# Performance work log

Measured on AMD Instinct MI355X. Metric: run time of the kernel, lower is better.

Reference implementation:

```python
import jax, jax.numpy as jnp
import numpy as np

M, N, D = 16384, 128, 2048  # actions, question tokens, ExpSet.dim


def setup_inputs() -> dict:
    key = jax.random.key(0)
    ks = jax.random.split(key, 6)
    s1 = 1.0 / np.sqrt(2 * D)  # torch Linear default init bounds
    s2 = 1.0 / np.sqrt(D)
    return {
        "action_embedding": jax.random.normal(ks[0], (M, D), jnp.float32),
        "question_t": jax.random.normal(ks[1], (N, D), jnp.float32),
        "history_t": jax.random.normal(ks[2], (D,), jnp.float32),
        "W1": jax.random.uniform(ks[3], (D, 2 * D), jnp.float32, -s1, s1),
        "b1": jnp.zeros((D,), jnp.float32),
        "W2": jax.random.uniform(ks[4], (D, D), jnp.float32, -s2, s2),
        "b2": jnp.zeros((D,), jnp.float32),
    }


def reference(action_embedding, question_t, history_t, W1, b1, W2, b2):
    # Attention: each action (query) attends over the n question tokens.
    # Equivalent to expand->attend->sum in the torch code, but without
    # materializing the [m, n, d] expanded tensor.
    scores = action_embedding @ question_t.T              # [M, N]
    attn = jax.nn.softmax(scores, axis=1)                 # softmax over tokens
    question = attn @ question_t                          # [M, D] (attended + summed)

    # Perceptron(2d -> d -> d) on cat([history, question])
    hist = jnp.broadcast_to(history_t, (action_embedding.shape[0], history_t.shape[0]))
    qh = jnp.concatenate([hist, question], axis=1)        # [M, 2D]
    h = jax.nn.relu(qh @ W1.T + b1)                       # [M, D]
    qwh = h @ W2.T + b2                                   # [M, D]

    # Elementwise dot with action embeddings, softmax over actions.
    semantic_scores = jnp.sum(qwh * action_embedding, axis=1)  # [M]
    return jax.nn.softmax(semantic_scores, axis=0)
```

## Files before the change

kernel.cpp:

```cpp
#include <hip/hip_runtime.h>
#include <hip/hip_bf16.h>


typedef _Float16 f16;
typedef __attribute__((ext_vector_type(8))) _Float16 half8;
typedef __attribute__((ext_vector_type(4))) _Float16 half4_t;
typedef __attribute__((ext_vector_type(4))) float f32x4;

#define GLL(gp, lp)                                                              \
  __builtin_amdgcn_global_load_lds(                                              \
      (const __attribute__((address_space(1))) void*)(gp),                       \
      (__attribute__((address_space(3))) void*)(lp), 16, 0, 0)

#define WAITN(n)                                                                 \
  do {                                                                           \
    asm volatile("s_waitcnt vmcnt(" #n ")" ::: "memory");                        \
    __builtin_amdgcn_sched_barrier(0);                                           \
  } while (0)

template <int NT, int LDA, int LDB>
__device__ __forceinline__ void kloop1(const f16* __restrict__ A,
                                       const f16* __restrict__ B,
                                       f16* __restrict__ SM,
                                       f32x4 (&acc)[4][4],
                                       int lane, int wv, int wm, int wn) {
  static_assert(NT >= 4, "depth-3 pipeline needs NT >= 4");
  const int f = lane & 15, kk = lane >> 4;
  const int cS = (lane & 7) ^ (lane >> 3);
  const int kkS = (cS & 3) * 8;
  const int rS = 2 * (lane >> 3) + (cS >> 2);
  const size_t offA0 = (size_t)(16 * (wv * 2 + 0) + rS) * LDA + kkS;
  const size_t offA1 = (size_t)(16 * (wv * 2 + 1) + rS) * LDA + kkS;
  const size_t offB0 = (size_t)(16 * (wv * 2 + 0) + rS) * LDB + kkS;
  const size_t offB1 = (size_t)(16 * (wv * 2 + 1) + rS) * LDB + kkS;
  const int Ld0 = (wv * 2 + 0) * 512, Ld1 = (wv * 2 + 1) * 512;

  int aoff[4], boff[4];
  #pragma unroll
  for (int mf = 0; mf < 4; ++mf) {
    const int R = wm + mf * 16 + f;
    const int c2 = (((R & 1) << 2) | kk) ^ ((R >> 1) & 7);
    aoff[mf] = (R >> 1) * 64 + c2 * 8;
  }
  #pragma unroll
  for (int nf = 0; nf < 4; ++nf) {
    const int R = wn + nf * 16 + f;
    const int c2 = (((R & 1) << 2) | kk) ^ ((R >> 1) & 7);
    boff[nf] = (R >> 1) * 64 + c2 * 8;
  }

  auto STAGE = [&](int set, int kt) {
    f16* base = SM + set * 8192;
    GLL(A + offA0 + kt, base + Ld0);
    GLL(A + offA1 + kt, base + Ld1);
    GLL(B + offB0 + kt, base + 4096 + Ld0);
    GLL(B + offB1 + kt, base + 4096 + Ld1);
  };
  auto COMPUTE = [&](int set) {
    const f16* p = SM + set * 8192;
    half8 a[4], b[4];
    #pragma unroll
    for (int mf = 0; mf < 4; ++mf) a[mf] = *(const half8*)&p[aoff[mf]];
    #pragma unroll
    for (int nf = 0; nf < 4; ++nf) b[nf] = *(const half8*)&p[4096 + boff[nf]];
    __builtin_amdgcn_s_setprio(1);
    #pragma unroll
    for (int mf = 0; mf < 4; ++mf)
      #pragma unroll
      for (int nf = 0; nf < 4; ++nf)
        acc[mf][nf] = __builtin_amdgcn_mfma_f32_16x16x32_f16(a[mf], b[nf], acc[mf][nf], 0, 0, 0);
    __builtin_amdgcn_s_setprio(0);
  };

  STAGE(0, 0);
  STAGE(1, 32);
  STAGE(2, 64);
  #pragma unroll 1
  for (int t = 0; t < NT - 3; ++t) {
    STAGE((t + 3) & 3, (t + 3) * 32);
    WAITN(12);
    __builtin_amdgcn_s_barrier();
    COMPUTE(t & 3);
    __builtin_amdgcn_s_barrier();
  }
  WAITN(8);
  __builtin_amdgcn_s_barrier();
  COMPUTE((NT - 3) & 3);
  __builtin_amdgcn_s_barrier();
  WAITN(4);
  __builtin_amdgcn_s_barrier();
  COMPUTE((NT - 2) & 3);
  __builtin_amdgcn_s_barrier();
  WAITN(0);
  __builtin_amdgcn_s_barrier();
  COMPUTE((NT - 1) & 3);
  __builtin_amdgcn_s_barrier();
}

template <int NT, int LDA, int LDB>
__device__ __forceinline__ void kloop256(const f16* __restrict__ A,
                                         const f16* __restrict__ B,
                                         f16* __restrict__ SM,
                                         f32x4 (&acc)[8][4],
                                         int lane, int wv, int wm, int wn) {
  static_assert(NT >= 4, "pipeline needs NT >= 4");
  const int f = lane & 15, kk = lane >> 4;
  const int cS = (lane & 7) ^ (lane >> 3);
  const int kkS = (cS & 3) * 8;
  const int rS = 2 * (lane >> 3) + (cS >> 2);
  const size_t offA0 = (size_t)(16 * (wv * 2 + 0) + rS) * LDA + kkS;
  const size_t offA1 = (size_t)(16 * (wv * 2 + 1) + rS) * LDA + kkS;
  const size_t offB0 = (size_t)(16 * (wv * 2 + 0) + rS) * LDB + kkS;
  const size_t offB1 = (size_t)(16 * (wv * 2 + 1) + rS) * LDB + kkS;
  const int Ld0 = (wv * 2 + 0) * 512, Ld1 = (wv * 2 + 1) * 512;

  int aoff[8], boff[4];
  #pragma unroll
  for (int mf = 0; mf < 8; ++mf) {
    const int R = wm + mf * 16 + f;
    const int c2 = (((R & 1) << 2) | kk) ^ ((R >> 1) & 7);
    aoff[mf] = (R >> 1) * 64 + c2 * 8;
  }
  #pragma unroll
  for (int nf = 0; nf < 4; ++nf) {
    const int R = wn + nf * 16 + f;
    const int c2 = (((R & 1) << 2) | kk) ^ ((R >> 1) & 7);
    boff[nf] = (R >> 1) * 64 + c2 * 8;
  }

  auto STAGE = [&](int set, int kt) {
    f16* base = SM + set * 16384;
    GLL(A + offA0 + kt, base + Ld0);
    GLL(A + offA1 + kt, base + Ld1);
    GLL(B + offB0 + kt, base + 8192 + Ld0);
    GLL(B + offB1 + kt, base + 8192 + Ld1);
  };
  auto COMPUTE = [&](int set) {
    const f16* p = SM + set * 16384;
    half8 a[8], b[4];
    #pragma unroll
    for (int mf = 0; mf < 8; ++mf) a[mf] = *(const half8*)&p[aoff[mf]];
    #pragma unroll
    for (int nf = 0; nf < 4; ++nf) b[nf] = *(const half8*)&p[8192 + boff[nf]];
    __builtin_amdgcn_s_setprio(1);
    #pragma unroll
    for (int mf = 0; mf < 8; ++mf)
      #pragma unroll
      for (int nf = 0; nf < 4; ++nf)
        acc[mf][nf] = __builtin_amdgcn_mfma_f32_16x16x32_f16(a[mf], b[nf], acc[mf][nf], 0, 0, 0);
    __builtin_amdgcn_s_setprio(0);
  };

  STAGE(0, 0);
  STAGE(1, 32);
  int cs = 0;
  #pragma unroll 1
  for (int t = 0; t < NT - 2; ++t) {
    int ss = cs + 2; if (ss >= 3) ss -= 3;
    STAGE(ss, (t + 2) * 32);
    WAITN(8);
    __builtin_amdgcn_s_barrier();
    COMPUTE(cs);
    __builtin_amdgcn_s_barrier();
    ++cs; if (cs == 3) cs = 0;
  }
  WAITN(4);
  __builtin_amdgcn_s_barrier();
  COMPUTE(cs);
  __builtin_amdgcn_s_barrier();
  ++cs; if (cs == 3) cs = 0;
  WAITN(0);
  __builtin_amdgcn_s_barrier();
  COMPUTE(cs);
  __builtin_amdgcn_s_barrier();
}


__global__ __launch_bounds__(256) void c_kernel(const float* __restrict__ W1,
                                                const float* __restrict__ b1,
                                                const float* __restrict__ hist,
                                                float* __restrict__ c) {
  const int wave = threadIdx.x >> 6, lane = threadIdx.x & 63;
  const int j = blockIdx.x * 4 + wave;
  const float* row = W1 + (size_t)j * 4096;
  float s = 0.f;
  #pragma unroll 2
  for (int kq = lane; kq < 512; kq += 64) {
    const float4 w = *(const float4*)&row[kq * 4];
    const float4 h = *(const float4*)&hist[kq * 4];
    s += w.x * h.x + w.y * h.y + w.z * h.z + w.w * h.w;
  }
  #pragma unroll
  for (int mask = 1; mask < 64; mask <<= 1) s += __shfl_xor(s, mask);
  if (lane == 0) c[j] = s + b1[j];
}

__device__ __forceinline__ half4_t f16hi4(const float4 v) {
  half4_t h;
  h.x = (f16)v.x; h.y = (f16)v.y; h.z = (f16)v.z; h.w = (f16)v.w;
  return h;
}

__global__ __launch_bounds__(256) void prep_AQ(const float* __restrict__ A,
                                               const float* __restrict__ Q,
                                               const float* __restrict__ b2,
                                               f16* __restrict__ Af,
                                               f16* __restrict__ Qf,
                                               float* __restrict__ ab2) {
  const int wv = threadIdx.x >> 6, lane = threadIdx.x & 63;
  if (blockIdx.x < 4096) {
    const size_t row = (size_t)blockIdx.x * 4 + wv;
    const float* ar = A + row * 2048;
    float dot = 0.f;
    #pragma unroll 2
    for (int c0 = 0; c0 < 2048; c0 += 256) {
      const int col = c0 + lane * 4;
      const float4 v = *(const float4*)&ar[col];
      const float4 bb = *(const float4*)&b2[col];
      dot += v.x * bb.x + v.y * bb.y + v.z * bb.z + v.w * bb.w;
      *(half4_t*)&Af[row * 2048 + col] = f16hi4(v);
    }
    #pragma unroll
    for (int mask = 1; mask < 64; mask <<= 1) dot += __shfl_xor(dot, mask);
    if (lane == 0) ab2[row] = dot;
  } else {
    const size_t row = (size_t)(blockIdx.x - 4096) * 4 + wv;
    const float* qr = Q + row * 2048;
    #pragma unroll 2
    for (int c0 = 0; c0 < 2048; c0 += 256) {
      const int col = c0 + lane * 4;
      const float4 v = *(const float4*)&qr[col];
      *(half4_t*)&Qf[row * 2048 + col] = f16hi4(v);
    }
  }
}

__global__ __launch_bounds__(256) void transpose_f16(const float* __restrict__ src,
                                                     int R, int C,
                                                     f16* __restrict__ dst) {
  __shared__ float T[64][65];
  const int c0 = blockIdx.x * 64, r0 = blockIdx.y * 64;
  const int t = threadIdx.x;
  {
    const int rl = t >> 4, cl = (t & 15) * 4;
    #pragma unroll
    for (int ii = 0; ii < 4; ++ii) {
      const float4 v = *(const float4*)&src[(size_t)(r0 + rl + ii * 16) * C + c0 + cl];
      T[rl + ii * 16][cl + 0] = v.x; T[rl + ii * 16][cl + 1] = v.y;
      T[rl + ii * 16][cl + 2] = v.z; T[rl + ii * 16][cl + 3] = v.w;
    }
  }
  __syncthreads();
  const int cc = t >> 2, rr0 = (t & 3) * 16;
  f16 u[16];
  #pragma unroll
  for (int k = 0; k < 16; ++k) u[k] = (f16)T[rr0 + k][cc];
  f16* ph = dst + (size_t)(c0 + cc) * R + r0 + rr0;
  #pragma unroll
  for (int k4 = 0; k4 < 4; ++k4)
    *(half4_t*)&ph[k4 * 4] = *(half4_t*)&u[k4 * 4];
}

template <int BM, int TM>
__global__ __launch_bounds__(256) void gemm_bt_f16(const float* __restrict__ A,
                                                   const float* __restrict__ B,
                                                   f16* __restrict__ C,
                                                   int K, int lda, int ldb, int ldc) {
  constexpr int BN = 64, BK = 32;
  constexpr int ASTR = BM + 12, BSTR = BN + 4;
  __shared__ float As[BK][ASTR];
  __shared__ float Bs[BK][BSTR];
  const int tid = threadIdx.x;
  const int tx = tid & 15, ty = tid >> 4;
  const int m0 = ty * TM, n0 = tx * 4;
  const size_t bm = (size_t)blockIdx.x * BM, bn = (size_t)blockIdx.y * BN;
  const float* Ab = A + bm * lda;
  const float* Bb = B + bn * ldb;
  float acc[TM][4];
  #pragma unroll
  for (int i = 0; i < TM; ++i)
    #pragma unroll
    for (int j = 0; j < 4; ++j) acc[i][j] = 0.f;
  for (int kt = 0; kt < K; kt += BK) {
    #pragma unroll
    for (int it = 0; it < BM * BK / 4 / 256; ++it) {
      const int idx = it * 256 + tid;
      const int row = idx >> 3, kq = idx & 7;
      const float4 v = *(const float4*)&Ab[(size_t)row * lda + kt + kq * 4];
      As[kq * 4 + 0][row] = v.x; As[kq * 4 + 1][row] = v.y;
      As[kq * 4 + 2][row] = v.z; As[kq * 4 + 3][row] = v.w;
    }
    #pragma unroll
    for (int it = 0; it < BN * BK / 4 / 256; ++it) {
      const int idx = it * 256 + tid;
      const int row = idx >> 3, kq = idx & 7;
      const float4 v = *(const float4*)&Bb[(size_t)row * ldb + kt + kq * 4];
      Bs[kq * 4 + 0][row] = v.x; Bs[kq * 4 + 1][row] = v.y;
      Bs[kq * 4 + 2][row] = v.z; Bs[kq * 4 + 3][row] = v.w;
    }
    __syncthreads();
    #pragma unroll
    for (int k = 0; k < BK; ++k) {
      float av[TM];
      #pragma unroll
      for (int i = 0; i < TM; ++i) av[i] = As[k][m0 + i];
      const float4 b = *(const float4*)&Bs[k][n0];
      const float bv[4] = {b.x, b.y, b.z, b.w};
      #pragma unroll
      for (int i = 0; i < TM; ++i)
        #pragma unroll
        for (int j = 0; j < 4; ++j) acc[i][j] = fmaf(av[i], bv[j], acc[i][j]);
    }
    __syncthreads();
  }
  #pragma unroll
  for (int i = 0; i < TM; ++i) {
    f16* crow = C + (bm + m0 + i) * (size_t)ldc + bn + n0;
    half4_t h;
    h.x = (f16)acc[i][0]; h.y = (f16)acc[i][1];
    h.z = (f16)acc[i][2]; h.w = (f16)acc[i][3];
    *(half4_t*)crow = h;
  }
}

__global__ __launch_bounds__(256, 2) void s_attn(const f16* __restrict__ Af,
                                                 const f16* __restrict__ Qf,
                                                 f16* __restrict__ at) {
  __shared__ f16 SM[32768];
  const int tid = threadIdx.x, lane = tid & 63, wv = tid >> 6;
  const int wm = (wv >> 1) * 64, wn = (wv & 1) * 64;
  const int f = lane & 15, kk = lane >> 4;
  const size_t bm = (size_t)blockIdx.x * 128;

  f32x4 acc[4][4];
  #pragma unroll
  for (int mf = 0; mf < 4; ++mf)
    #pragma unroll
    for (int nf = 0; nf < 4; ++nf) acc[mf][nf] = 0.f;

  kloop1<64, 2048, 2048>(Af + bm * 2048, Qf, SM, acc, lane, wv, wm, wn);

  float* sred = (float*)SM;
  float* ssum = sred + 256;
  const int rowbase = wm + kk * 4;
  float rmax[4][4];
  #pragma unroll
  for (int mf = 0; mf < 4; ++mf)
    #pragma unroll
    for (int r = 0; r < 4; ++r) {
      float m4 = fmaxf(fmaxf(acc[mf][0][r], acc[mf][1][r]),
                       fmaxf(acc[mf][2][r], acc[mf][3][r]));
      m4 = fmaxf(m4, __shfl_xor(m4, 1));
      m4 = fmaxf(m4, __shfl_xor(m4, 2));
      m4 = fmaxf(m4, __shfl_xor(m4, 4));
      m4 = fmaxf(m4, __shfl_xor(m4, 8));
      rmax[mf][r] = m4;
    }
  if (f == 0) {
    #pragma unroll
    for (int mf = 0; mf < 4; ++mf)
      #pragma unroll
      for (int r = 0; r < 4; ++r)
        sred[(rowbase + mf * 16 + r) * 2 + (wv & 1)] = rmax[mf][r];
  }
  __syncthreads();
  #pragma unroll
  for (int mf = 0; mf < 4; ++mf)
    #pragma unroll
    for (int r = 0; r < 4; ++r) {
      const int row = rowbase + mf * 16 + r;
      rmax[mf][r] = fmaxf(sred[row * 2], sred[row * 2 + 1]);
    }
  float rsum[4][4];
  #pragma unroll
  for (int mf = 0; mf < 4; ++mf)
    #pragma unroll
    for (int r = 0; r < 4; ++r) {
      float s = 0.f;
      #pragma unroll
      for (int nf = 0; nf < 4; ++nf) {
        acc[mf][nf][r] = __expf(acc[mf][nf][r] - rmax[mf][r]);
        s += acc[mf][nf][r];
      }
      s += __shfl_xor(s, 1);
      s += __shfl_xor(s, 2);
      s += __shfl_xor(s, 4);
      s += __shfl_xor(s, 8);
      rsum[mf][r] = s;
    }
  if (f == 0) {
    #pragma unroll
    for (int mf = 0; mf < 4; ++mf)
      #pragma unroll
      for (int r = 0; r < 4; ++r)
        ssum[(rowbase + mf * 16 + r) * 2 + (wv & 1)] = rsum[mf][r];
  }
  __syncthreads();
  #pragma unroll
  for (int mf = 0; mf < 4; ++mf)
    #pragma unroll
    for (int r = 0; r < 4; ++r) {
      const int row = rowbase + mf * 16 + r;
      const float inv = 1.0f / (ssum[row * 2] + ssum[row * 2 + 1]);
      const size_t orow = (bm + row) * 128;
      #pragma unroll
      for (int nf = 0; nf < 4; ++nf)
        at[orow + wn + nf * 16 + f] = (f16)(acc[mf][nf][r] * inv);
    }
}

__global__ __launch_bounds__(256, 2) void h_kernel(const f16* __restrict__ at,
                                                   const f16* __restrict__ QWt,
                                                   const float* __restrict__ cvec,
                                                   f16* __restrict__ H) {
  __shared__ f16 SM[32768];
  const int tid = threadIdx.x, lane = tid & 63, wv = tid >> 6;
  const int wm = (wv >> 1) * 64, wn = (wv & 1) * 64;
  const int f = lane & 15, kk = lane >> 4;
  const size_t bm = (size_t)(blockIdx.x & 127) * 128;
  const size_t bn = (size_t)(blockIdx.x >> 7) * 128;

  f32x4 acc[4][4];
  #pragma unroll
  for (int mf = 0; mf < 4; ++mf)
    #pragma unroll
    for (int nf = 0; nf < 4; ++nf) acc[mf][nf] = 0.f;

  kloop1<4, 128, 128>(at + bm * 128, QWt + bn * 128, SM, acc, lane, wv, wm, wn);

  float ccv[4];
  #pragma unroll
  for (int nf = 0; nf < 4; ++nf) ccv[nf] = cvec[bn + wn + nf * 16 + f];
  #pragma unroll
  for (int mf = 0; mf < 4; ++mf)
    #pragma unroll
    for (int r = 0; r < 4; ++r) {
      const size_t row = bm + wm + mf * 16 + kk * 4 + r;
      #pragma unroll
      for (int nf = 0; nf < 4; ++nf)
        H[row * 2048 + bn + wn + nf * 16 + f] =
            (f16)fmaxf(acc[mf][nf][r] + ccv[nf], 0.f);
    }
}

__global__ __launch_bounds__(512, 1) void fused_g(
    const f16* __restrict__ Af, const f16* __restrict__ H,
    const f16* __restrict__ W2t, float* __restrict__ partial) {
  extern __shared__ f16 SM[];
  const int tid = threadIdx.x, lane = tid & 63, wv = tid >> 6;
  const int wm = (wv >> 2) * 128, wn = (wv & 3) * 64;
  const int f = lane & 15, kk = lane >> 4;
  const int lin = blockIdx.x;
  const int sid = (lin & 7) * 64 + (lin >> 3);
  const int bmI = sid & 63, bnI = sid >> 6;
  const size_t bm = (size_t)bmI * 256;
  const size_t bn = (size_t)bnI * 256;

  f32x4 acc[8][4];
  #pragma unroll
  for (int mf = 0; mf < 8; ++mf)
    #pragma unroll
    for (int nf = 0; nf < 4; ++nf) acc[mf][nf] = 0.f;

  kloop256<64, 2048, 2048>(Af + bm * 2048, W2t + bn * 2048, SM, acc, lane, wv, wm, wn);

  float part[8][4];
  #pragma unroll
  for (int mf = 0; mf < 8; ++mf)
    #pragma unroll
    for (int r = 0; r < 4; ++r) {
      const size_t hrow = (bm + wm + mf * 16 + kk * 4 + r) * 2048 + bn + wn + f;
      float s = 0.f;
      #pragma unroll
      for (int nf = 0; nf < 4; ++nf)
        s += (float)H[hrow + nf * 16] * acc[mf][nf][r];
      part[mf][r] = s;
    }
  #pragma unroll
  for (int mf = 0; mf < 8; ++mf)
    #pragma unroll
    for (int r = 0; r < 4; ++r) {
      part[mf][r] += __shfl_xor(part[mf][r], 1);
      part[mf][r] += __shfl_xor(part[mf][r], 2);
      part[mf][r] += __shfl_xor(part[mf][r], 4);
      part[mf][r] += __shfl_xor(part[mf][r], 8);
    }
  if (f == 0) {
    const size_t slab = (size_t)(bnI * 4 + (wv & 3)) * 16384;
    #pragma unroll
    for (int mf = 0; mf < 8; ++mf)
      #pragma unroll
      for (int r = 0; r < 4; ++r)
        partial[slab + bm + wm + mf * 16 + kk * 4 + r] = part[mf][r];
  }
}


__global__ __launch_bounds__(256) void k_sem(const float* __restrict__ partial,
                                             const float* __restrict__ ab2,
                                             float* __restrict__ semantic,
                                             float* __restrict__ bstats) {
  const int m = blockIdx.x * 256 + threadIdx.x;
  float s = ab2[m];
  #pragma unroll
  for (int nb = 0; nb < 32; ++nb) s += partial[(size_t)nb * 16384 + m];
  semantic[m] = s;
  float mx = s;
  #pragma unroll
  for (int mask = 1; mask < 64; mask <<= 1) mx = fmaxf(mx, __shfl_xor(mx, mask));
  __shared__ float wmax[4], wsum[4];
  const int wave = threadIdx.x >> 6, lane = threadIdx.x & 63;
  if (lane == 0) wmax[wave] = mx;
  __syncthreads();
  const float bmax = fmaxf(fmaxf(wmax[0], wmax[1]), fmaxf(wmax[2], wmax[3]));
  float e = expf(s - bmax);
  #pragma unroll
  for (int mask = 1; mask < 64; mask <<= 1) e += __shfl_xor(e, mask);
  if (lane == 0) wsum[wave] = e;
  __syncthreads();
  if (threadIdx.x == 0) {
    bstats[blockIdx.x * 2] = bmax;
    bstats[blockIdx.x * 2 + 1] = wsum[0] + wsum[1] + wsum[2] + wsum[3];
  }
}

__global__ __launch_bounds__(256) void k_out(const float* __restrict__ semantic,
                                             const float* __restrict__ bstats,
                                             float* __restrict__ out) {
  __shared__ float g0s, g1s;
  const int tid = threadIdx.x;
  if (tid < 64) {
    const float bm = bstats[tid * 2], bs = bstats[tid * 2 + 1];
    float gm = bm;
    #pragma unroll
    for (int mask = 1; mask < 64; mask <<= 1) gm = fmaxf(gm, __shfl_xor(gm, mask));
    float gs = bs * expf(bm - gm);
    #pragma unroll
    for (int mask = 1; mask < 64; mask <<= 1) gs += __shfl_xor(gs, mask);
    if (tid == 0) { g0s = gm; g1s = gs; }
  }
  __syncthreads();
  const int m = blockIdx.x * 256 + tid;
  out[m] = expf(semantic[m] - g0s) / g1s;
}


extern "C" void kernel_launch(void* const* d_in, const int* in_sizes, int n_in,
                              void* d_out, int out_size, void* d_ws, size_t ws_size,
                              hipStream_t stream) {
  (void)in_sizes; (void)n_in; (void)out_size; (void)ws_size;
  const float* A    = (const float*)d_in[0];
  const float* Q    = (const float*)d_in[1];
  const float* hist = (const float*)d_in[2];
  const float* W1   = (const float*)d_in[3];
  const float* b1   = (const float*)d_in[4];
  const float* W2   = (const float*)d_in[5];
  const float* b2   = (const float*)d_in[6];
  float* out = (float*)d_out;

  char* ws = (char*)d_ws;
  f16* Af      = (f16*)ws;   ws += (size_t)16384 * 2048 * 2;
  f16* Hbuf    = (f16*)ws;   ws += (size_t)16384 * 2048 * 2;
  f16* W2t     = (f16*)ws;   ws += (size_t)2048 * 2048 * 2;
  f16* Qf      = (f16*)ws;   ws += (size_t)128 * 2048 * 2;
  f16* QWt     = (f16*)ws;   ws += (size_t)2048 * 128 * 2;
  f16* at      = (f16*)ws;   ws += (size_t)16384 * 128 * 2;
  float* c_vec = (float*)ws; ws += 2048 * 4;
  float* ab2   = (float*)ws; ws += 16384 * 4;
  float* partial  = (float*)ws; ws += (size_t)32 * 16384 * 4;
  float* semantic = (float*)ws; ws += 16384 * 4;
  float* bstats   = (float*)ws; ws += 128 * 4;

  hipFuncSetAttribute((const void*)fused_g,
                      hipFuncAttributeMaxDynamicSharedMemorySize, 98304);

  c_kernel<<<512, 256, 0, stream>>>(W1, b1, hist, c_vec);
  gemm_bt_f16<32, 2><<<dim3(64, 2), 256, 0, stream>>>(W1 + 2048, Q, QWt,
                                                      2048, 4096, 2048, 128);
  transpose_f16<<<dim3(32, 32), 256, 0, stream>>>(W2, 2048, 2048, W2t);
  prep_AQ<<<4128, 256, 0, stream>>>(A, Q, b2, Af, Qf, ab2);
  s_attn<<<128, 256, 0, stream>>>(Af, Qf, at);
  h_kernel<<<2048, 256, 0, stream>>>(at, QWt, c_vec, Hbuf);
  fused_g<<<512, 512, 98304, stream>>>(Af, Hbuf, W2t, partial);
  k_sem<<<64, 256, 0, stream>>>(partial, ab2, semantic, bstats);
  k_out<<<64, 256, 0, stream>>>(semantic, bstats, out);
}
```

Measured before the change: 325.2 us.

## Split-K the QW GEMM and deepen the fused_g LDS pipeline to four stages

The small W1·Q GEMM launched only 128 blocks. It now splits K into 8 slabs across blockIdx.z, writing fp32 partials that a new combine kernel sums and converts to f16, so more of the GPU is busy. In kloop256 the 3-stage LDS ring becomes 4 stages with power-of-two indexing, and fused_g's dynamic LDS grows to 128 KiB. This drops the trailing barrier after each compute step. The split-K path adds an extra kernel launch and about 8 MB of partial traffic, and the larger LDS may reduce fused_g occupancy.

```diff
diff --git a/kernel.cpp b/kernel.cpp
--- a/kernel.cpp
+++ b/kernel.cpp
@@ -103,7 +103,7 @@
                                          f16* __restrict__ SM,
                                          f32x4 (&acc)[8][4],
                                          int lane, int wv, int wm, int wn) {
-  static_assert(NT >= 4, "pipeline needs NT >= 4");
+  static_assert(NT >= 3, "pipeline needs NT >= 3");
   const int f = lane & 15, kk = lane >> 4;
   const int cS = (lane & 7) ^ (lane >> 3);
   const int kkS = (cS & 3) * 8;
@@ -153,26 +153,19 @@
 
   STAGE(0, 0);
   STAGE(1, 32);
-  int cs = 0;
   #pragma unroll 1
   for (int t = 0; t < NT - 2; ++t) {
-    int ss = cs + 2; if (ss >= 3) ss -= 3;
-    STAGE(ss, (t + 2) * 32);
+    STAGE((t + 2) & 3, (t + 2) * 32);
     WAITN(8);
     __builtin_amdgcn_s_barrier();
-    COMPUTE(cs);
-    __builtin_amdgcn_s_barrier();
-    ++cs; if (cs == 3) cs = 0;
+    COMPUTE(t & 3);
   }
   WAITN(4);
   __builtin_amdgcn_s_barrier();
-  COMPUTE(cs);
-  __builtin_amdgcn_s_barrier();
-  ++cs; if (cs == 3) cs = 0;
+  COMPUTE((NT - 2) & 3);
   WAITN(0);
   __builtin_amdgcn_s_barrier();
-  COMPUTE(cs);
-  __builtin_amdgcn_s_barrier();
+  COMPUTE((NT - 1) & 3);
 }
 
 
@@ -262,10 +255,11 @@
 }
 
 template <int BM, int TM>
-__global__ __launch_bounds__(256) void gemm_bt_f16(const float* __restrict__ A,
-                                                   const float* __restrict__ B,
-                                                   f16* __restrict__ C,
-                                                   int K, int lda, int ldb, int ldc) {
+__global__ __launch_bounds__(256) void gemm_bt_sk(const float* __restrict__ A,
+                                                  const float* __restrict__ B,
+                                                  float* __restrict__ Cpart,
+                                                  int Kslab, int lda, int ldb,
+                                                  int ldc, int M) {
   constexpr int BN = 64, BK = 32;
   constexpr int ASTR = BM + 12, BSTR = BN + 4;
   __shared__ float As[BK][ASTR];
@@ -274,6 +268,7 @@
   const int tx = tid & 15, ty = tid >> 4;
   const int m0 = ty * TM, n0 = tx * 4;
   const size_t bm = (size_t)blockIdx.x * BM, bn = (size_t)blockIdx.y * BN;
+  const int kb = blockIdx.z * Kslab;
   const float* Ab = A + bm * lda;
   const float* Bb = B + bn * ldb;
   float acc[TM][4];
@@ -281,7 +276,7 @@
   for (int i = 0; i < TM; ++i)
     #pragma unroll
     for (int j = 0; j < 4; ++j) acc[i][j] = 0.f;
-  for (int kt = 0; kt < K; kt += BK) {
+  for (int kt = kb; kt < kb + Kslab; kt += BK) {
     #pragma unroll
     for (int it = 0; it < BM * BK / 4 / 256; ++it) {
       const int idx = it * 256 + tid;
@@ -313,14 +308,25 @@
     }
     __syncthreads();
   }
+  float* base = Cpart + (size_t)blockIdx.z * M * ldc;
   #pragma unroll
   for (int i = 0; i < TM; ++i) {
-    f16* crow = C + (bm + m0 + i) * (size_t)ldc + bn + n0;
-    half4_t h;
-    h.x = (f16)acc[i][0]; h.y = (f16)acc[i][1];
-    h.z = (f16)acc[i][2]; h.w = (f16)acc[i][3];
-    *(half4_t*)crow = h;
-  }
+    float* crow = base + (bm + m0 + i) * (size_t)ldc + bn + n0;
+    #pragma unroll
+    for (int j = 0; j < 4; ++j) crow[j] = acc[i][j];
+  }
+}
+
+__global__ __launch_bounds__(256) void qwt_combine(const float* __restrict__ part,
+                                                   f16* __restrict__ QWt) {
+  const size_t i = ((size_t)blockIdx.x * 256 + threadIdx.x) * 4;
+  float4 s = make_float4(0.f, 0.f, 0.f, 0.f);
+  #pragma unroll
+  for (int z = 0; z < 8; ++z) {
+    const float4 v = *(const float4*)&part[(size_t)z * 262144 + i];
+    s.x += v.x; s.y += v.y; s.z += v.z; s.w += v.w;
+  }
+  *(half4_t*)&QWt[i] = f16hi4(s);
 }
 
 __global__ __launch_bounds__(256, 2) void s_attn(const f16* __restrict__ Af,
@@ -565,6 +571,7 @@
   f16* Qf      = (f16*)ws;   ws += (size_t)128 * 2048 * 2;
   f16* QWt     = (f16*)ws;   ws += (size_t)2048 * 128 * 2;
   f16* at      = (f16*)ws;   ws += (size_t)16384 * 128 * 2;
+  float* qwt_part = (float*)ws; ws += (size_t)8 * 2048 * 128 * 4;
   float* c_vec = (float*)ws; ws += 2048 * 4;
   float* ab2   = (float*)ws; ws += 16384 * 4;
   float* partial  = (float*)ws; ws += (size_t)32 * 16384 * 4;
@@ -572,16 +579,17 @@
   float* bstats   = (float*)ws; ws += 128 * 4;
 
   hipFuncSetAttribute((const void*)fused_g,
-                      hipFuncAttributeMaxDynamicSharedMemorySize, 98304);
+                      hipFuncAttributeMaxDynamicSharedMemorySize, 131072);
 
   c_kernel<<<512, 256, 0, stream>>>(W1, b1, hist, c_vec);
-  gemm_bt_f16<32, 2><<<dim3(64, 2), 256, 0, stream>>>(W1 + 2048, Q, QWt,
-                                                      2048, 4096, 2048, 128);
+  gemm_bt_sk<32, 2><<<dim3(64, 2, 8), 256, 0, stream>>>(W1 + 2048, Q, qwt_part,
+                                                        256, 4096, 2048, 128, 2048);
+  qwt_combine<<<256, 256, 0, stream>>>(qwt_part, QWt);
   transpose_f16<<<dim3(32, 32), 256, 0, stream>>>(W2, 2048, 2048, W2t);
   prep_AQ<<<4128, 256, 0, stream>>>(A, Q, b2, Af, Qf, ab2);
   s_attn<<<128, 256, 0, stream>>>(Af, Qf, at);
   h_kernel<<<2048, 256, 0, stream>>>(at, QWt, c_vec, Hbuf);
-  fused_g<<<512, 512, 98304, stream>>>(Af, Hbuf, W2t, partial);
+  fused_g<<<512, 512, 131072, stream>>>(Af, Hbuf, W2t, partial);
   k_sem<<<64, 256, 0, stream>>>(partial, ab2, semantic, bstats);
   k_out<<<64, 256, 0, stream>>>(semantic, bstats, out);
 }
```

Result: faster. 272.4 us (-16.2%).
